# Optimization experiments

Measured on AMD Instinct MI355X. Metric: run time of the kernel, lower is better.

## Reference

```python
import jax, jax.numpy as jnp
import numpy as np

FWD_W = 1.0
BWD_W = 1.0
EPS = 1e-12  # guard sqrt gradient at exact zero


def setup_inputs() -> dict:
    key = jax.random.key(0)
    k1, k2 = jax.random.split(key)
    pred = jax.random.normal(k1, (4, 8192, 3), dtype=jnp.float32)
    target = jax.random.normal(k2, (4, 8192, 3), dtype=jnp.float32)
    return {"pred": pred, "target": target}


def reference(pred, target):
    # pairwise Euclidean distances (torch.cdist, p=2): (B, N, M)
    sq = (jnp.sum(pred * pred, axis=-1)[:, :, None]
          + jnp.sum(target * target, axis=-1)[:, None, :]
          - 2.0 * jnp.einsum('bnd,bmd->bnm', pred, target))
    dist = jnp.sqrt(jnp.maximum(sq, EPS))
    forward_dist = jnp.min(dist, axis=2)   # (B, N): pred -> nearest target
    backward_dist = jnp.min(dist, axis=1)  # (B, M): target -> nearest pred
    total = FWD_W * jnp.sum(forward_dist, axis=1) + BWD_W * jnp.sum(backward_dist, axis=1)
    return jnp.mean(total)  # reduction='mean'
```

## Files before the change

### kernel.cpp

```cpp
#include <hip/hip_runtime.h>
#include <math.h>

#define BATCH   4
#define NPTS    8192
#define THREADS 256
#define QPT     16
#define QPB     (THREADS * QPT)
#define QBLK    (NPTS / QPB)
#define NCHUNK  32
#define SLICE   (NPTS / NCHUNK)
#define NQTOT   (2 * BATCH * NPTS)
#define PART_ELEMS ((size_t)NCHUNK * NQTOT)

typedef float v2f __attribute__((ext_vector_type(2)));


static __device__ __forceinline__ v2f pk_fma_b_lo(v2f a, v2f b, v2f c) {
    v2f d;
    asm("v_pk_fma_f32 %0, %1, %2, %3 op_sel:[0,0,0] op_sel_hi:[1,0,1]"
        : "=v"(d) : "v"(a), "v"(b), "v"(c));
    return d;
}
static __device__ __forceinline__ v2f pk_fma_b_hi(v2f a, v2f b, v2f c) {
    v2f d;
    asm("v_pk_fma_f32 %0, %1, %2, %3 op_sel:[0,1,0] op_sel_hi:[1,1,1]"
        : "=v"(d) : "v"(a), "v"(b), "v"(c));
    return d;
}
static __device__ __forceinline__ v2f pk_fma_b_lo_c_hi(v2f a, v2f b, v2f c) {
    v2f d;
    asm("v_pk_fma_f32 %0, %1, %2, %3 op_sel:[0,0,1] op_sel_hi:[1,0,1]"
        : "=v"(d) : "v"(a), "v"(b), "v"(c));
    return d;
}
static __device__ __forceinline__ float min3f(float a, float b, float c) {
    float d;
    asm("v_min3_f32 %0, %1, %2, %3" : "=v"(d) : "v"(a), "v"(b), "v"(c));
    return d;
}

__global__ __launch_bounds__(THREADS)
void chamfer_min_kernel(const float* __restrict__ pred,
                        const float* __restrict__ target,
                        _Float16* __restrict__ partial)
{
    __shared__ float4 sdb[SLICE];

    const int tid = threadIdx.x;
    const int bid = blockIdx.x;
    const int c   = bid & (NCHUNK - 1);
    const int qb  = (bid >> 5) & (QBLK - 1);
    const int b   = (bid >> 6) & 3;
    const int dir = bid >> 8;

    const float* __restrict__ qsrc = (dir == 0) ? pred : target;
    const float* __restrict__ dsrc = (dir == 0) ? target : pred;

    {
        const float* dbase = dsrc + ((size_t)b * NPTS + (size_t)c * SLICE) * 3;
        const float x = dbase[3 * tid + 0];
        const float y = dbase[3 * tid + 1];
        const float z = dbase[3 * tid + 2];
        sdb[tid] = make_float4(-2.0f * x, -2.0f * y, -2.0f * z,
                               fmaf(x, x, fmaf(y, y, z * z)));
    }

    v2f qx[8], qy[8], qz[8];
    float qq[QPT];
    {
        const float* qbase = qsrc + ((size_t)b * NPTS + (size_t)qb * QPB) * 3;
        #pragma unroll
        for (int p = 0; p < 8; ++p) {
            const int i0 = (2 * p + 0) * THREADS + tid;
            const int i1 = (2 * p + 1) * THREADS + tid;
            const float x0 = qbase[3 * i0 + 0], y0 = qbase[3 * i0 + 1], z0 = qbase[3 * i0 + 2];
            const float x1 = qbase[3 * i1 + 0], y1 = qbase[3 * i1 + 1], z1 = qbase[3 * i1 + 2];
            qx[p] = (v2f){x0, x1};
            qy[p] = (v2f){y0, y1};
            qz[p] = (v2f){z0, z1};
            qq[2 * p + 0] = fmaf(x0, x0, fmaf(y0, y0, z0 * z0));
            qq[2 * p + 1] = fmaf(x1, x1, fmaf(y1, y1, z1 * z1));
        }
    }

    __syncthreads();

    float mn[QPT];
    #pragma unroll
    for (int i = 0; i < QPT; ++i) mn[i] = 3.0e38f;

    #pragma unroll 1
    for (int j = 0; j < SLICE; j += 4) {
        const float4 d0 = sdb[j + 0];
        const float4 d1 = sdb[j + 1];
        const float4 d2 = sdb[j + 2];
        const float4 d3 = sdb[j + 3];
        const v2f a0 = (v2f){d0.x, d0.y}, b0 = (v2f){d0.z, d0.w};
        const v2f a1 = (v2f){d1.x, d1.y}, b1 = (v2f){d1.z, d1.w};
        const v2f a2 = (v2f){d2.x, d2.y}, b2 = (v2f){d2.z, d2.w};
        const v2f a3 = (v2f){d3.x, d3.y}, b3 = (v2f){d3.z, d3.w};

        #pragma unroll
        for (int p = 0; p < 8; ++p) {
            const v2f s0 = pk_fma_b_lo(qx[p], a0, pk_fma_b_hi(qy[p], a0, pk_fma_b_lo_c_hi(qz[p], b0, b0)));
            const v2f s1 = pk_fma_b_lo(qx[p], a1, pk_fma_b_hi(qy[p], a1, pk_fma_b_lo_c_hi(qz[p], b1, b1)));
            const v2f s2 = pk_fma_b_lo(qx[p], a2, pk_fma_b_hi(qy[p], a2, pk_fma_b_lo_c_hi(qz[p], b2, b2)));
            const v2f s3 = pk_fma_b_lo(qx[p], a3, pk_fma_b_hi(qy[p], a3, pk_fma_b_lo_c_hi(qz[p], b3, b3)));
            mn[2 * p + 0] = min3f(mn[2 * p + 0], s0.x, s1.x);
            mn[2 * p + 0] = min3f(mn[2 * p + 0], s2.x, s3.x);
            mn[2 * p + 1] = min3f(mn[2 * p + 1], s0.y, s1.y);
            mn[2 * p + 1] = min3f(mn[2 * p + 1], s2.y, s3.y);
        }
    }

    const int region = (dir * BATCH + b) * QBLK + qb;
    _Float16* dst = partial + (size_t)c * NQTOT + (size_t)region * QPB;
    #pragma unroll
    for (int i = 0; i < QPT; ++i) {
        dst[i * THREADS + tid] = (_Float16)fmaxf(qq[i] + mn[i], 1e-12f);
    }
}

__global__ __launch_bounds__(256)
void chamfer_reduce1(const _Float16* __restrict__ partial,
                     float* __restrict__ bsum)
{
    const int tid = threadIdx.x;
    const int t   = blockIdx.x * 256 + tid;

    float m = 3.0e38f;
    #pragma unroll
    for (int c = 0; c < NCHUNK; ++c) {
        m = fminf(m, (float)partial[(size_t)c * NQTOT + t]);
    }
    float acc = sqrtf(m);

    #pragma unroll
    for (int off = 32; off > 0; off >>= 1)
        acc += __shfl_down(acc, off, 64);

    __shared__ float wsum[4];
    if ((tid & 63) == 0) wsum[tid >> 6] = acc;
    __syncthreads();
    if (tid == 0) bsum[blockIdx.x] = wsum[0] + wsum[1] + wsum[2] + wsum[3];
}

__global__ __launch_bounds__(256)
void chamfer_reduce2(const float* __restrict__ bsum,
                     float* __restrict__ out)
{
    const int tid = threadIdx.x;
    float v = bsum[tid];
    #pragma unroll
    for (int off = 32; off > 0; off >>= 1)
        v += __shfl_down(v, off, 64);

    __shared__ float wsum[4];
    if ((tid & 63) == 0) wsum[tid >> 6] = v;
    __syncthreads();
    if (tid == 0) out[0] = (wsum[0] + wsum[1] + wsum[2] + wsum[3]) * (1.0f / BATCH);
}

extern "C" void kernel_launch(void* const* d_in, const int* in_sizes, int n_in,
                              void* d_out, int out_size, void* d_ws, size_t ws_size,
                              hipStream_t stream)
{
    const float* pred   = (const float*)d_in[0];
    const float* target = (const float*)d_in[1];
    float* out          = (float*)d_out;
    _Float16* partial   = (_Float16*)d_ws;
    float* bsum         = (float*)((char*)d_ws + PART_ELEMS * sizeof(_Float16));

    const int nblocks = 2 * BATCH * QBLK * NCHUNK;
    chamfer_min_kernel<<<nblocks, THREADS, 0, stream>>>(pred, target, partial);
    chamfer_reduce1<<<NQTOT / 256, 256, 0, stream>>>(partial, bsum);
    chamfer_reduce2<<<1, 256, 0, stream>>>(bsum, out);
}
```

Before: 98.05 us.

## Compute pairwise distance cross terms with split-fp16 MFMA instead of packed FP32 FMA

Moves the inner distance computation onto 32x32x16 fp16 matrix-core instructions. Each coordinate is split into high and low fp16 parts so the dot product plus the database norm is recovered to near fp32 accuracy. A new transform kernel precomputes the fp16 database fragments. The target dimension is split into two halves instead of 32 chunks, which shrinks the partial buffer, and the query norm, clamp and sqrt now happen in the reduction. This trades FP32 VALU work for MFMA throughput, at the cost of an extra launch, cross-lane shuffle reductions and possible precision loss from the fp16 split.

```diff
diff --git a/kernel.cpp b/kernel.cpp
--- a/kernel.cpp
+++ b/kernel.cpp
@@ -4,136 +4,153 @@
 #define BATCH   4
 #define NPTS    8192
 #define THREADS 256
-#define QPT     16
-#define QPB     (THREADS * QPT)
-#define QBLK    (NPTS / QPB)
-#define NCHUNK  32
-#define SLICE   (NPTS / NCHUNK)
 #define NQTOT   (2 * BATCH * NPTS)
-#define PART_ELEMS ((size_t)NCHUNK * NQTOT)
-
-typedef float v2f __attribute__((ext_vector_type(2)));
-
-
-static __device__ __forceinline__ v2f pk_fma_b_lo(v2f a, v2f b, v2f c) {
-    v2f d;
-    asm("v_pk_fma_f32 %0, %1, %2, %3 op_sel:[0,0,0] op_sel_hi:[1,0,1]"
-        : "=v"(d) : "v"(a), "v"(b), "v"(c));
-    return d;
-}
-static __device__ __forceinline__ v2f pk_fma_b_hi(v2f a, v2f b, v2f c) {
-    v2f d;
-    asm("v_pk_fma_f32 %0, %1, %2, %3 op_sel:[0,1,0] op_sel_hi:[1,1,1]"
-        : "=v"(d) : "v"(a), "v"(b), "v"(c));
-    return d;
-}
-static __device__ __forceinline__ v2f pk_fma_b_lo_c_hi(v2f a, v2f b, v2f c) {
-    v2f d;
-    asm("v_pk_fma_f32 %0, %1, %2, %3 op_sel:[0,0,1] op_sel_hi:[1,0,1]"
-        : "=v"(d) : "v"(a), "v"(b), "v"(c));
-    return d;
-}
-static __device__ __forceinline__ float min3f(float a, float b, float c) {
-    float d;
-    asm("v_min3_f32 %0, %1, %2, %3" : "=v"(d) : "v"(a), "v"(b), "v"(c));
-    return d;
-}
+#define CHUNK   1024
+#define TSPLIT  2
+#define THALF   (NPTS / TSPLIT)
+#define NCHUNKS (THALF / CHUNK)
+
+typedef _Float16 h8  __attribute__((ext_vector_type(8)));
+typedef float    f16v __attribute__((ext_vector_type(16)));
 
 __global__ __launch_bounds__(THREADS)
+void chamfer_transform(const float* __restrict__ pred,
+                       const float* __restrict__ target,
+                       h8* __restrict__ trans_lo,
+                       h8* __restrict__ trans_hi)
+{
+    const int p   = blockIdx.x * THREADS + threadIdx.x;
+    const int arr = p >> 15;
+    const int pb  = p & 32767;
+
+    const float* src = (arr ? target : pred) + (size_t)pb * 3;
+    const float x = src[0], y = src[1], z = src[2];
+
+    const _Float16 hx = (_Float16)x;  const float lxf = x - (float)hx;
+    const _Float16 hy = (_Float16)y;  const float lyf = y - (float)hy;
+    const _Float16 hz = (_Float16)z;  const float lzf = z - (float)hz;
+    const _Float16 lx = (_Float16)lxf, ly = (_Float16)lyf, lz = (_Float16)lzf;
+
+    const float tx = (float)hx + (float)lx;
+    const float ty = (float)hy + (float)ly;
+    const float tz = (float)hz + (float)lz;
+    const float tt = fmaf(tx, tx, fmaf(ty, ty, tz * tz));
+    const _Float16 tth = (_Float16)tt;
+    const _Float16 ttl = (_Float16)(tt - (float)tth);
+
+    const _Float16 n2 = (_Float16)(-2.0f);
+    h8 lo = { n2 * hx, n2 * hy, n2 * hz, tth,
+              n2 * hx, n2 * hy, n2 * hz, ttl };
+    h8 hi = { n2 * lx, n2 * ly, n2 * lz, (_Float16)0.0f,
+              (_Float16)0.0f, (_Float16)0.0f, (_Float16)0.0f, (_Float16)0.0f };
+
+    trans_lo[p] = lo;
+    trans_hi[p] = hi;
+}
+
+__global__ __launch_bounds__(THREADS, 4)
 void chamfer_min_kernel(const float* __restrict__ pred,
                         const float* __restrict__ target,
-                        _Float16* __restrict__ partial)
-{
-    __shared__ float4 sdb[SLICE];
-
+                        const h8* __restrict__ trans_lo,
+                        const h8* __restrict__ trans_hi,
+                        float* __restrict__ partial)
+{
+    __shared__ uint4 slo[CHUNK];
+    __shared__ uint4 shi[CHUNK];
+
+    const int tid  = threadIdx.x;
+    const int lane = tid & 63;
+    const int wave = tid >> 6;
+    const int n    = lane & 31;
+    const int hi   = lane >> 5;
+
+    const int bid = blockIdx.x;
+    const int ts  = bid & 1;
+    const int qg  = (bid >> 1) & 63;
+    const int b   = (bid >> 7) & 3;
+    const int dir = bid >> 9;
+
+    const int  qtbase = qg * 128 + wave * 32;
+    const int  tbase  = ts * THALF;
+    const int  darr   = (dir == 0) ? 1 : 0;
+    const float* qraw = ((dir == 0) ? pred : target) + (size_t)b * NPTS * 3;
+
+    h8 afrag;
+    {
+        const float* qp = qraw + (size_t)(qtbase + n) * 3;
+        const float x = qp[0], y = qp[1], z = qp[2];
+        const _Float16 hx = (_Float16)x; const _Float16 lx = (_Float16)(x - (float)hx);
+        const _Float16 hy = (_Float16)y; const _Float16 ly = (_Float16)(y - (float)hy);
+        const _Float16 hz = (_Float16)z; const _Float16 lz = (_Float16)(z - (float)hz);
+        const _Float16 one  = (_Float16)1.0f;
+        const _Float16 zero = (_Float16)0.0f;
+        if (hi == 0) afrag = (h8){hx, hy, hz, one, lx, ly, lz, one};
+        else         afrag = (h8){hx, hy, hz, zero, zero, zero, zero, zero};
+    }
+
+    float mn[16];
+    #pragma unroll
+    for (int i = 0; i < 16; ++i) mn[i] = 3.0e38f;
+
+    const size_t gbase = (size_t)(darr * 4 + b) * NPTS + tbase;
+    const h8* bsrc = hi ? (const h8*)shi : (const h8*)slo;
+
+    for (int c = 0; c < NCHUNKS; ++c) {
+        const size_t cb = gbase + (size_t)c * CHUNK;
+        #pragma unroll
+        for (int r = 0; r < 4; ++r) {
+            slo[r * THREADS + tid] = ((const uint4*)trans_lo)[cb + r * THREADS + tid];
+            shi[r * THREADS + tid] = ((const uint4*)trans_hi)[cb + r * THREADS + tid];
+        }
+        __syncthreads();
+
+        #pragma unroll 2
+        for (int t = 0; t < CHUNK / 32; ++t) {
+            const h8 bfrag = bsrc[t * 32 + n];
+            f16v zc = {};
+            const f16v d = __builtin_amdgcn_mfma_f32_32x32x16_f16(afrag, bfrag, zc, 0, 0, 0);
+            #pragma unroll
+            for (int i = 0; i < 16; ++i) mn[i] = fminf(mn[i], d[i]);
+        }
+        __syncthreads();
+    }
+
+    #pragma unroll
+    for (int mask = 1; mask <= 16; mask <<= 1) {
+        #pragma unroll
+        for (int i = 0; i < 16; ++i)
+            mn[i] = fminf(mn[i], __shfl_xor(mn[i], mask, 64));
+    }
+
+    if (n == 0) {
+        float* dst = partial + (size_t)ts * NQTOT
+                   + (size_t)(dir * 4 + b) * NPTS + qtbase;
+        #pragma unroll
+        for (int i = 0; i < 16; ++i) {
+            const int row = (i & 3) + 8 * (i >> 2) + 4 * hi;
+            dst[row] = mn[i];
+        }
+    }
+}
+
+__global__ __launch_bounds__(THREADS)
+void chamfer_reduce1(const float* __restrict__ partial,
+                     const float* __restrict__ pred,
+                     const float* __restrict__ target,
+                     float* __restrict__ bsum)
+{
     const int tid = threadIdx.x;
-    const int bid = blockIdx.x;
-    const int c   = bid & (NCHUNK - 1);
-    const int qb  = (bid >> 5) & (QBLK - 1);
-    const int b   = (bid >> 6) & 3;
-    const int dir = bid >> 8;
-
-    const float* __restrict__ qsrc = (dir == 0) ? pred : target;
-    const float* __restrict__ dsrc = (dir == 0) ? target : pred;
-
-    {
-        const float* dbase = dsrc + ((size_t)b * NPTS + (size_t)c * SLICE) * 3;
-        const float x = dbase[3 * tid + 0];
-        const float y = dbase[3 * tid + 1];
-        const float z = dbase[3 * tid + 2];
-        sdb[tid] = make_float4(-2.0f * x, -2.0f * y, -2.0f * z,
-                               fmaf(x, x, fmaf(y, y, z * z)));
-    }
-
-    v2f qx[8], qy[8], qz[8];
-    float qq[QPT];
-    {
-        const float* qbase = qsrc + ((size_t)b * NPTS + (size_t)qb * QPB) * 3;
-        #pragma unroll
-        for (int p = 0; p < 8; ++p) {
-            const int i0 = (2 * p + 0) * THREADS + tid;
-            const int i1 = (2 * p + 1) * THREADS + tid;
-            const float x0 = qbase[3 * i0 + 0], y0 = qbase[3 * i0 + 1], z0 = qbase[3 * i0 + 2];
-            const float x1 = qbase[3 * i1 + 0], y1 = qbase[3 * i1 + 1], z1 = qbase[3 * i1 + 2];
-            qx[p] = (v2f){x0, x1};
-            qy[p] = (v2f){y0, y1};
-            qz[p] = (v2f){z0, z1};
-            qq[2 * p + 0] = fmaf(x0, x0, fmaf(y0, y0, z0 * z0));
-            qq[2 * p + 1] = fmaf(x1, x1, fmaf(y1, y1, z1 * z1));
-        }
-    }
-
-    __syncthreads();
-
-    float mn[QPT];
-    #pragma unroll
-    for (int i = 0; i < QPT; ++i) mn[i] = 3.0e38f;
-
-    #pragma unroll 1
-    for (int j = 0; j < SLICE; j += 4) {
-        const float4 d0 = sdb[j + 0];
-        const float4 d1 = sdb[j + 1];
-        const float4 d2 = sdb[j + 2];
-        const float4 d3 = sdb[j + 3];
-        const v2f a0 = (v2f){d0.x, d0.y}, b0 = (v2f){d0.z, d0.w};
-        const v2f a1 = (v2f){d1.x, d1.y}, b1 = (v2f){d1.z, d1.w};
-        const v2f a2 = (v2f){d2.x, d2.y}, b2 = (v2f){d2.z, d2.w};
-        const v2f a3 = (v2f){d3.x, d3.y}, b3 = (v2f){d3.z, d3.w};
-
-        #pragma unroll
-        for (int p = 0; p < 8; ++p) {
-            const v2f s0 = pk_fma_b_lo(qx[p], a0, pk_fma_b_hi(qy[p], a0, pk_fma_b_lo_c_hi(qz[p], b0, b0)));
-            const v2f s1 = pk_fma_b_lo(qx[p], a1, pk_fma_b_hi(qy[p], a1, pk_fma_b_lo_c_hi(qz[p], b1, b1)));
-            const v2f s2 = pk_fma_b_lo(qx[p], a2, pk_fma_b_hi(qy[p], a2, pk_fma_b_lo_c_hi(qz[p], b2, b2)));
-            const v2f s3 = pk_fma_b_lo(qx[p], a3, pk_fma_b_hi(qy[p], a3, pk_fma_b_lo_c_hi(qz[p], b3, b3)));
-            mn[2 * p + 0] = min3f(mn[2 * p + 0], s0.x, s1.x);
-            mn[2 * p + 0] = min3f(mn[2 * p + 0], s2.x, s3.x);
-            mn[2 * p + 1] = min3f(mn[2 * p + 1], s0.y, s1.y);
-            mn[2 * p + 1] = min3f(mn[2 * p + 1], s2.y, s3.y);
-        }
-    }
-
-    const int region = (dir * BATCH + b) * QBLK + qb;
-    _Float16* dst = partial + (size_t)c * NQTOT + (size_t)region * QPB;
-    #pragma unroll
-    for (int i = 0; i < QPT; ++i) {
-        dst[i * THREADS + tid] = (_Float16)fmaxf(qq[i] + mn[i], 1e-12f);
-    }
-}
-
-__global__ __launch_bounds__(256)
-void chamfer_reduce1(const _Float16* __restrict__ partial,
-                     float* __restrict__ bsum)
-{
-    const int tid = threadIdx.x;
-    const int t   = blockIdx.x * 256 + tid;
-
-    float m = 3.0e38f;
-    #pragma unroll
-    for (int c = 0; c < NCHUNK; ++c) {
-        m = fminf(m, (float)partial[(size_t)c * NQTOT + t]);
-    }
-    float acc = sqrtf(m);
+    const int i   = blockIdx.x * THREADS + tid;
+
+    const float m = fminf(partial[i], partial[NQTOT + i]);
+
+    const int dir  = i >> 15;
+    const int rest = i & 32767;
+    const float* qp = ((dir == 0) ? pred : target) + (size_t)rest * 3;
+    const float x = qp[0], y = qp[1], z = qp[2];
+    const float qq = fmaf(x, x, fmaf(y, y, z * z));
+
+    float acc = sqrtf(fmaxf(qq + m, 1e-12f));
 
     #pragma unroll
     for (int off = 32; off > 0; off >>= 1)
@@ -145,7 +162,7 @@
     if (tid == 0) bsum[blockIdx.x] = wsum[0] + wsum[1] + wsum[2] + wsum[3];
 }
 
-__global__ __launch_bounds__(256)
+__global__ __launch_bounds__(THREADS)
 void chamfer_reduce2(const float* __restrict__ bsum,
                      float* __restrict__ out)
 {
@@ -168,11 +185,20 @@
     const float* pred   = (const float*)d_in[0];
     const float* target = (const float*)d_in[1];
     float* out          = (float*)d_out;
-    _Float16* partial   = (_Float16*)d_ws;
-    float* bsum         = (float*)((char*)d_ws + PART_ELEMS * sizeof(_Float16));
-
-    const int nblocks = 2 * BATCH * QBLK * NCHUNK;
-    chamfer_min_kernel<<<nblocks, THREADS, 0, stream>>>(pred, target, partial);
-    chamfer_reduce1<<<NQTOT / 256, 256, 0, stream>>>(partial, bsum);
-    chamfer_reduce2<<<1, 256, 0, stream>>>(bsum, out);
-}
+
+    h8*    trans_lo = (h8*)d_ws;
+    h8*    trans_hi = (h8*)((char*)d_ws + (size_t)65536 * 16);
+    float* partial  = (float*)((char*)d_ws + (size_t)131072 * 16);
+    float* bsum     = partial + 2 * NQTOT;
+
+    chamfer_transform<<<NQTOT / THREADS / 1, THREADS, 0, stream>>>(
+        pred, target, trans_lo, trans_hi);
+
+    chamfer_min_kernel<<<2 * BATCH * 64 * TSPLIT, THREADS, 0, stream>>>(
+        pred, target, trans_lo, trans_hi, partial);
+
+    chamfer_reduce1<<<NQTOT / THREADS, THREADS, 0, stream>>>(
+        partial, pred, target, bsum);
+
+    chamfer_reduce2<<<1, THREADS, 0, stream>>>(bsum, out);
+}
```

After: 82.82 us. 1.18x faster.
